# Kernel optimization log

Hardware: AMD Instinct MI355X
Metric: run time of the kernel (lower is better)

## Reference

```python
import jax, jax.numpy as jnp
import numpy as np

N_BITS = 13  # ceil(log2(8192))
D_MODEL = 1024


def setup_inputs() -> dict:
    key = jax.random.key(0)
    k1, k2 = jax.random.split(key)
    x = jax.random.randint(k1, (4, 8192), 0, 8192, dtype=jnp.int64 if jax.config.jax_enable_x64 else jnp.int32)
    emb = jax.random.normal(k2, (N_BITS, D_MODEL), dtype=jnp.float32)
    # __init__ L2-normalizes embedding rows
    emb = emb / jnp.linalg.norm(emb, axis=1, keepdims=True)
    return {"x": x, "emb": emb}


def reference(x, emb):
    # bit decomposition: mask[..., b] = bit b of x  -> shape (*x.shape, n_bits)
    bits = jnp.arange(N_BITS, dtype=x.dtype)
    mask = ((x[..., None] >> bits) & 1).astype(emb.dtype)
    # out[i] = sum_{b: bit b set} emb[b]  ==  mask @ emb
    return jnp.einsum('...b,bd->...d', mask, emb)
```

## Files before the change

kernel.cpp:

```cpp
#include <hip/hip_runtime.h>

#define NBITS 13
#define DMODEL 1024
#define PPB 32

typedef float v4f __attribute__((ext_vector_type(4)));

__global__ __launch_bounds__(256) void bpe_kernel(const int* __restrict__ x,
                                                  const float* __restrict__ emb,
                                                  float* __restrict__ out,
                                                  int npos) {
    const int t = threadIdx.x;

    v4f frag[NBITS];
#pragma unroll
    for (int b = 0; b < NBITS; ++b) {
        frag[b] = *reinterpret_cast<const v4f*>(emb + b * DMODEL + t * 4);
    }

    const int base = blockIdx.x * PPB;

    if (base + PPB <= npos) {
        int xv[PPB];
#pragma unroll
        for (int i = 0; i < PPB; i += 4) {
            const int4 v = *reinterpret_cast<const int4*>(x + base + i);
            xv[i + 0] = v.x;
            xv[i + 1] = v.y;
            xv[i + 2] = v.z;
            xv[i + 3] = v.w;
        }

        float* o = out + (size_t)base * DMODEL + (size_t)(t * 4);
#pragma unroll
        for (int i = 0; i < PPB; ++i) {
            const int v = xv[i];
            v4f acc = {0.f, 0.f, 0.f, 0.f};
#pragma unroll
            for (int b = 0; b < NBITS; ++b) {
                const float m = __int_as_float(((v >> b) & 1) ? 0x3f800000 : 0);
                acc.x = fmaf(m, frag[b].x, acc.x);
                acc.y = fmaf(m, frag[b].y, acc.y);
                acc.z = fmaf(m, frag[b].z, acc.z);
                acc.w = fmaf(m, frag[b].w, acc.w);
            }
            *reinterpret_cast<v4f*>(o + (size_t)i * DMODEL) = acc;
        }
    } else {
        for (int p = base; p < npos; ++p) {
            const int v = x[p];
            v4f acc = {0.f, 0.f, 0.f, 0.f};
#pragma unroll
            for (int b = 0; b < NBITS; ++b) {
                const float m = __int_as_float(((v >> b) & 1) ? 0x3f800000 : 0);
                acc.x = fmaf(m, frag[b].x, acc.x);
                acc.y = fmaf(m, frag[b].y, acc.y);
                acc.z = fmaf(m, frag[b].z, acc.z);
                acc.w = fmaf(m, frag[b].w, acc.w);
            }
            *reinterpret_cast<v4f*>(out + (size_t)p * DMODEL + (size_t)(t * 4)) = acc;
        }
    }
}

extern "C" void kernel_launch(void* const* d_in, const int* in_sizes, int n_in,
                              void* d_out, int out_size, void* d_ws, size_t ws_size,
                              hipStream_t stream) {
    const int* x = (const int*)d_in[0];
    const float* emb = (const float*)d_in[1];
    float* out = (float*)d_out;

    const int npos = in_sizes[0];

    const int grid = (npos + PPB - 1) / PPB;
    bpe_kernel<<<grid, 256, 0, stream>>>(x, emb, out, npos);
}
```

Measured before the change: 27.57 us.

## Replace per-bit FMA sum with two-table split LUT lookup

Builds a 192-row lookup table in workspace (128 rows holding every combination of the low 7 bits, 64 rows for the high 6 bits), then produces each output row as the sum of two table rows. The per-position 13-step FMA chain becomes two vector loads and an add. The cost is an extra kernel launch, a 768KB table write, and table reads that should mostly hit cache. PPB is halved to 16, and a fallback direct kernel runs when the workspace is too small.

```diff
diff --git a/kernel.cpp b/kernel.cpp
--- a/kernel.cpp
+++ b/kernel.cpp
@@ -2,23 +2,50 @@
 
 #define NBITS 13
 #define DMODEL 1024
-#define PPB 32
+#define PPB 16
+#define LUT_LO 128
+#define LUT_HI 64
+#define LUT_ROWS (LUT_LO + LUT_HI)
 
 typedef float v4f __attribute__((ext_vector_type(4)));
 
-__global__ __launch_bounds__(256) void bpe_kernel(const int* __restrict__ x,
-                                                  const float* __restrict__ emb,
-                                                  float* __restrict__ out,
-                                                  int npos) {
+__global__ __launch_bounds__(256) void lut_build(const float* __restrict__ emb,
+                                                 float* __restrict__ lut) {
+    const int r = blockIdx.x;
     const int t = threadIdx.x;
+    v4f acc = {0.f, 0.f, 0.f, 0.f};
+    if (r < LUT_LO) {
+#pragma unroll
+        for (int b = 0; b < 7; ++b) {
+            const float m = __int_as_float(((r >> b) & 1) ? 0x3f800000 : 0);
+            const v4f e = *reinterpret_cast<const v4f*>(emb + b * DMODEL + t * 4);
+            acc.x = fmaf(m, e.x, acc.x);
+            acc.y = fmaf(m, e.y, acc.y);
+            acc.z = fmaf(m, e.z, acc.z);
+            acc.w = fmaf(m, e.w, acc.w);
+        }
+    } else {
+        const int v = r - LUT_LO;
+#pragma unroll
+        for (int b = 0; b < 6; ++b) {
+            const float m = __int_as_float(((v >> b) & 1) ? 0x3f800000 : 0);
+            const v4f e = *reinterpret_cast<const v4f*>(emb + (7 + b) * DMODEL + t * 4);
+            acc.x = fmaf(m, e.x, acc.x);
+            acc.y = fmaf(m, e.y, acc.y);
+            acc.z = fmaf(m, e.z, acc.z);
+            acc.w = fmaf(m, e.w, acc.w);
+        }
+    }
+    *reinterpret_cast<v4f*>(lut + (size_t)r * DMODEL + t * 4) = acc;
+}
 
-    v4f frag[NBITS];
-#pragma unroll
-    for (int b = 0; b < NBITS; ++b) {
-        frag[b] = *reinterpret_cast<const v4f*>(emb + b * DMODEL + t * 4);
-    }
-
+__global__ __launch_bounds__(256) void bpe_lut_kernel(const int* __restrict__ x,
+                                                      const float* __restrict__ lut,
+                                                      float* __restrict__ out,
+                                                      int npos) {
+    const int t = threadIdx.x;
     const int base = blockIdx.x * PPB;
+    const float* hi = lut + (size_t)LUT_LO * DMODEL;
 
     if (base + PPB <= npos) {
         int xv[PPB];
@@ -30,36 +57,52 @@
             xv[i + 2] = v.z;
             xv[i + 3] = v.w;
         }
-
         float* o = out + (size_t)base * DMODEL + (size_t)(t * 4);
 #pragma unroll
         for (int i = 0; i < PPB; ++i) {
             const int v = xv[i];
-            v4f acc = {0.f, 0.f, 0.f, 0.f};
-#pragma unroll
-            for (int b = 0; b < NBITS; ++b) {
-                const float m = __int_as_float(((v >> b) & 1) ? 0x3f800000 : 0);
-                acc.x = fmaf(m, frag[b].x, acc.x);
-                acc.y = fmaf(m, frag[b].y, acc.y);
-                acc.z = fmaf(m, frag[b].z, acc.z);
-                acc.w = fmaf(m, frag[b].w, acc.w);
-            }
-            *reinterpret_cast<v4f*>(o + (size_t)i * DMODEL) = acc;
+            const v4f a = *reinterpret_cast<const v4f*>(
+                lut + (size_t)(v & (LUT_LO - 1)) * DMODEL + t * 4);
+            const v4f b = *reinterpret_cast<const v4f*>(
+                hi + (size_t)(v >> 7) * DMODEL + t * 4);
+            const v4f s = a + b;
+            *reinterpret_cast<v4f*>(o + (size_t)i * DMODEL) = s;
         }
     } else {
         for (int p = base; p < npos; ++p) {
             const int v = x[p];
-            v4f acc = {0.f, 0.f, 0.f, 0.f};
+            const v4f a = *reinterpret_cast<const v4f*>(
+                lut + (size_t)(v & (LUT_LO - 1)) * DMODEL + t * 4);
+            const v4f b = *reinterpret_cast<const v4f*>(
+                hi + (size_t)(v >> 7) * DMODEL + t * 4);
+            const v4f s = a + b;
+            *reinterpret_cast<v4f*>(out + (size_t)p * DMODEL + (size_t)(t * 4)) = s;
+        }
+    }
+}
+
+__global__ __launch_bounds__(256) void bpe_direct_kernel(const int* __restrict__ x,
+                                                         const float* __restrict__ emb,
+                                                         float* __restrict__ out,
+                                                         int npos) {
+    const int t = threadIdx.x;
+    v4f frag[NBITS];
 #pragma unroll
-            for (int b = 0; b < NBITS; ++b) {
-                const float m = __int_as_float(((v >> b) & 1) ? 0x3f800000 : 0);
-                acc.x = fmaf(m, frag[b].x, acc.x);
-                acc.y = fmaf(m, frag[b].y, acc.y);
-                acc.z = fmaf(m, frag[b].z, acc.z);
-                acc.w = fmaf(m, frag[b].w, acc.w);
-            }
-            *reinterpret_cast<v4f*>(out + (size_t)p * DMODEL + (size_t)(t * 4)) = acc;
+    for (int b = 0; b < NBITS; ++b) {
+        frag[b] = *reinterpret_cast<const v4f*>(emb + b * DMODEL + t * 4);
+    }
+    for (int p = blockIdx.x; p < npos; p += gridDim.x) {
+        const int v = x[p];
+        v4f acc = {0.f, 0.f, 0.f, 0.f};
+#pragma unroll
+        for (int b = 0; b < NBITS; ++b) {
+            const float m = __int_as_float(((v >> b) & 1) ? 0x3f800000 : 0);
+            acc.x = fmaf(m, frag[b].x, acc.x);
+            acc.y = fmaf(m, frag[b].y, acc.y);
+            acc.z = fmaf(m, frag[b].z, acc.z);
+            acc.w = fmaf(m, frag[b].w, acc.w);
         }
+        *reinterpret_cast<v4f*>(out + (size_t)p * DMODEL + (size_t)(t * 4)) = acc;
     }
 }
 
@@ -69,9 +112,16 @@
     const int* x = (const int*)d_in[0];
     const float* emb = (const float*)d_in[1];
     float* out = (float*)d_out;
-
     const int npos = in_sizes[0];
 
-    const int grid = (npos + PPB - 1) / PPB;
-    bpe_kernel<<<grid, 256, 0, stream>>>(x, emb, out, npos);
+    const size_t lut_bytes = (size_t)LUT_ROWS * DMODEL * sizeof(float);
+    if (ws_size >= lut_bytes) {
+        float* lut = (float*)d_ws;
+        lut_build<<<LUT_ROWS, 256, 0, stream>>>(emb, lut);
+        const int grid = (npos + PPB - 1) / PPB;
+        bpe_lut_kernel<<<grid, 256, 0, stream>>>(x, lut, out, npos);
+    } else {
+        int grid = npos < 2048 ? npos : 2048;
+        bpe_direct_kernel<<<grid, 256, 0, stream>>>(x, emb, out, npos);
+    }
 }
```

After: 32.05 us. 16.2% more time.
